# Optimization experiments

Hardware: AMD Instinct MI355X
Metric: run time of the kernel (lower is better)

The kernel has to match this reference:

```python
import jax, jax.numpy as jnp
from jax import lax
import numpy as np

LBDA = 0.1


def otam_cum_dist(dists, lbda=LBDA):
    """OTAM cumulative distance, dists: [Q, S, L, M] -> [Q, S].

    Matches the torch reference: pad last dim by 1 on each side with zeros,
    then run the banded soft-min (temperature lbda) DP recurrence. We use
    logaddexp for the stable form of -lbda*log(sum(exp(-x/lbda))).
    """
    Q, S, L, M = dists.shape
    d = jnp.pad(dists, ((0, 0), (0, 0), (0, 0), (1, 1)))  # [Q,S,L,M+2]

    # Row 0: cum[0,0]=0, cum[0,m]=sum_{k=1..m} d[0,k]  (prefix sum)
    zero_col = jnp.zeros((Q, S, 1), d.dtype)
    row0 = jnp.concatenate([zero_col, jnp.cumsum(d[:, :, 0, 1:], axis=-1)], axis=-1)

    # For m = 1 .. M+1: boundary columns (m==1 and m==M+1) add the
    # extra exp(-cum[l-1, m]/lbda) term.
    is_bnd = np.zeros(M + 1, dtype=bool)
    is_bnd[0] = True
    is_bnd[-1] = True
    is_bnd = jnp.asarray(is_bnd)

    def row_step(prev_row, d_row):
        # prev_row, d_row: [Q, S, M+2]
        def col_step(prev_cur, xs):
            d_lm, pr_m1, pr_m, bnd = xs  # each [Q,S] (bnd scalar)
            s = jnp.logaddexp(-pr_m1 / lbda, -prev_cur / lbda)
            s = jnp.where(bnd, jnp.logaddexp(s, -pr_m / lbda), s)
            cur = d_lm - lbda * s
            return cur, cur

        xs = (
            jnp.moveaxis(d_row[:, :, 1:], -1, 0),        # d[l, m],     m=1..M+1
            jnp.moveaxis(prev_row[:, :, :-1], -1, 0),    # cum[l-1,m-1]
            jnp.moveaxis(prev_row[:, :, 1:], -1, 0),     # cum[l-1,m]
            is_bnd,
        )
        zero = jnp.zeros(d_row.shape[:2], d_row.dtype)
        _, cols = lax.scan(col_step, zero, xs)           # [M+1, Q, S]
        new_row = jnp.concatenate([zero[..., None], jnp.moveaxis(cols, 0, -1)], axis=-1)
        return new_row, None

    d_rows = jnp.moveaxis(d[:, :, 1:, :], 2, 0)          # [L-1, Q, S, M+2]
    last_row, _ = lax.scan(row_step, row0, d_rows)
    return last_row[:, :, -1]


def setup_inputs() -> dict:
    key = jax.random.key(0)
    similarity = jax.random.uniform(key, (400, 400, 16, 16), dtype=jnp.float32)
    return {"similarity": similarity}


def reference(similarity):
    distance = 1.0 - similarity
    votes = otam_cum_dist(distance) + otam_cum_dist(
        jnp.transpose(distance, (0, 1, 3, 2))
    )
    votes = votes * 0.5
    return -votes
```

## Files before the change

### kernel.cpp

```cpp
#include <hip/hip_runtime.h>


#define KSC  14.426950408889634f
#define HCL2 0.034657359027997264f

#define A0 0.00013544f
#define A1 1.4369229f
#define A2 -0.67162489f
#define A3 0.31367219f
#define A4 -0.07916012f

#if __has_builtin(__builtin_amdgcn_exp2f)
static __device__ __forceinline__ float fexp2(float x) { return __builtin_amdgcn_exp2f(x); }
#else
static __device__ __forceinline__ float fexp2(float x) {
    float r; asm("v_exp_f32 %0, %1" : "=v"(r) : "v"(x)); return r;
}
#endif

static __device__ __forceinline__ float lse2(float x, float y) {
    float e = fexp2(-fabsf(x - y));
    float p = __builtin_fmaf(__builtin_fmaf(__builtin_fmaf(
                  __builtin_fmaf(A4, e, A3), e, A2), e, A1), e, A0);
    return fmaxf(x, y) + p;
}
static __device__ __forceinline__ float lse3(float x, float y, float z) {
    return lse2(lse2(x, y), z);
}

#define UNPACKK(rk, b0, b1, b2, b3)                                              \
    rk[0]=(b0.x-1.0f)*KSC;  rk[1]=(b0.y-1.0f)*KSC;  rk[2]=(b0.z-1.0f)*KSC;       \
    rk[3]=(b0.w-1.0f)*KSC;  rk[4]=(b1.x-1.0f)*KSC;  rk[5]=(b1.y-1.0f)*KSC;       \
    rk[6]=(b1.z-1.0f)*KSC;  rk[7]=(b1.w-1.0f)*KSC;  rk[8]=(b2.x-1.0f)*KSC;       \
    rk[9]=(b2.y-1.0f)*KSC;  rk[10]=(b2.z-1.0f)*KSC; rk[11]=(b2.w-1.0f)*KSC;      \
    rk[12]=(b3.x-1.0f)*KSC; rk[13]=(b3.y-1.0f)*KSC; rk[14]=(b3.z-1.0f)*KSC;      \
    rk[15]=(b3.w-1.0f)*KSC

#define PIPE_ADVANCE(l)                                                          \
    b0 = c0; b1 = c1; b2 = c2; b3 = c3;                                          \
    c0 = e0; c1 = e1; c2 = e2; c3 = e3;                                          \
    if ((l) + 2 < 16) {                                                          \
        e0 = tp[((l) + 2) * 4 + 0]; e1 = tp[((l) + 2) * 4 + 1];                  \
        e2 = tp[((l) + 2) * 4 + 2]; e3 = tp[((l) + 2) * 4 + 3];                  \
    }

__global__ __launch_bounds__(128) void otam_kernel(const float* __restrict__ sim,
                                                   float* __restrict__ out,
                                                   int npairs) {
    __shared__ float tshare[64];
    const int lane = threadIdx.x & 63;
    const int wid  = threadIdx.x >> 6;
    int p = blockIdx.x * 64 + lane;
    if (p >= npairs) p = npairs - 1;
    const float4* tp = (const float4*)(sim + (size_t)p * 256);

    float rk[16];
    float4 b0 = tp[0], b1 = tp[1], b2 = tp[2],  b3 = tp[3];
    float4 c0 = tp[4], c1 = tp[5], c2 = tp[6],  c3 = tp[7];
    float4 e0 = tp[8], e1 = tp[9], e2 = tp[10], e3 = tp[11];

    UNPACKK(rk, b0, b1, b2, b3);

    float resu;
    if (wid == 0) {
        float up[18];
        up[0] = 0.0f;
#pragma unroll
        for (int m = 1; m <= 16; ++m) up[m] = up[m - 1] + rk[m - 1];
        up[17] = up[16];

        for (int l = 1; l < 16; ++l) {
            PIPE_ADVANCE(l);
            UNPACKK(rk, b0, b1, b2, b3);
            float t   = up[1];
            float cur = lse2(1.0f, t) + rk[0];
            up[1] = cur;
            float a_old = t;
#pragma unroll
            for (int m = 2; m <= 16; ++m) {
                t      = up[m];
                cur    = lse2(a_old, cur) + rk[m - 1];
                up[m]  = cur;
                a_old  = t;
            }
            up[17] = lse3(a_old, cur, up[17]);
        }
        resu = up[17];
    } else {
        float S[16];
        {
            float cur = rk[0];
            S[0] = cur;
#pragma unroll
            for (int i = 1; i < 16; ++i) {
                cur  = lse2(1.0f, cur) + rk[i];
                S[i] = cur;
            }
        }
        for (int l = 1; l < 16; ++l) {
            PIPE_ADVANCE(l);
            UNPACKK(rk, b0, b1, b2, b3);
            float po  = S[0];
            float cur = S[0] + rk[0];
            S[0] = cur;
#pragma unroll
            for (int i = 1; i < 16; ++i) {
                float t = S[i];
                cur  = lse2(po, t) + rk[i];
                S[i] = cur;
                po   = t;
            }
        }
        {
            float po = S[0], cur = S[0];
#pragma unroll
            for (int i = 1; i < 16; ++i) {
                float t = S[i];
                cur = lse3(po, t, cur);
                po  = t;
            }
            tshare[lane] = cur;
        }
        resu = 0.0f;
    }

    __syncthreads();
    if (wid == 0) {
        out[p] = HCL2 * (resu + tshare[lane]);
    }
}

extern "C" void kernel_launch(void* const* d_in, const int* in_sizes, int n_in,
                              void* d_out, int out_size, void* d_ws, size_t ws_size,
                              hipStream_t stream) {
    const float* sim = (const float*)d_in[0];
    float* out       = (float*)d_out;
    int npairs = in_sizes[0] / 256;
    int blocks = (npairs + 63) / 64;
    otam_kernel<<<blocks, 128, 0, stream>>>(sim, out, npairs);
}
```

Measured before the change: 236.8 us.

## Stage inputs through double-buffered LDS with coalesced loads shared by both waves

Replaces per-lane strided global loads (each wave reading the full pair matrix) with cooperative coalesced float4 loads by all 128 threads into a padded, double-buffered shared memory staging area, processed two rows per chunk. This targets uncoalesced access and the duplicated global reads between the row-pass and column-pass waves. It adds a block barrier per chunk and shared memory usage, which may reduce occupancy.

```diff
diff --git a/kernel.cpp b/kernel.cpp
--- a/kernel.cpp
+++ b/kernel.cpp
@@ -28,105 +28,171 @@
     return lse2(lse2(x, y), z);
 }
 
-#define UNPACKK(rk, b0, b1, b2, b3)                                              \
-    rk[0]=(b0.x-1.0f)*KSC;  rk[1]=(b0.y-1.0f)*KSC;  rk[2]=(b0.z-1.0f)*KSC;       \
-    rk[3]=(b0.w-1.0f)*KSC;  rk[4]=(b1.x-1.0f)*KSC;  rk[5]=(b1.y-1.0f)*KSC;       \
-    rk[6]=(b1.z-1.0f)*KSC;  rk[7]=(b1.w-1.0f)*KSC;  rk[8]=(b2.x-1.0f)*KSC;       \
-    rk[9]=(b2.y-1.0f)*KSC;  rk[10]=(b2.z-1.0f)*KSC; rk[11]=(b2.w-1.0f)*KSC;      \
-    rk[12]=(b3.x-1.0f)*KSC; rk[13]=(b3.y-1.0f)*KSC; rk[14]=(b3.z-1.0f)*KSC;      \
-    rk[15]=(b3.w-1.0f)*KSC
-
-#define PIPE_ADVANCE(l)                                                          \
-    b0 = c0; b1 = c1; b2 = c2; b3 = c3;                                          \
-    c0 = e0; c1 = e1; c2 = e2; c3 = e3;                                          \
-    if ((l) + 2 < 16) {                                                          \
-        e0 = tp[((l) + 2) * 4 + 0]; e1 = tp[((l) + 2) * 4 + 1];                  \
-        e2 = tp[((l) + 2) * 4 + 2]; e3 = tp[((l) + 2) * 4 + 3];                  \
-    }
+#define UNPACKQ(rk, q)                                                         \
+    rk[0]=(q[0].x-1.0f)*KSC;  rk[1]=(q[0].y-1.0f)*KSC;                         \
+    rk[2]=(q[0].z-1.0f)*KSC;  rk[3]=(q[0].w-1.0f)*KSC;                         \
+    rk[4]=(q[1].x-1.0f)*KSC;  rk[5]=(q[1].y-1.0f)*KSC;                         \
+    rk[6]=(q[1].z-1.0f)*KSC;  rk[7]=(q[1].w-1.0f)*KSC;                         \
+    rk[8]=(q[2].x-1.0f)*KSC;  rk[9]=(q[2].y-1.0f)*KSC;                         \
+    rk[10]=(q[2].z-1.0f)*KSC; rk[11]=(q[2].w-1.0f)*KSC;                        \
+    rk[12]=(q[3].x-1.0f)*KSC; rk[13]=(q[3].y-1.0f)*KSC;                        \
+    rk[14]=(q[3].z-1.0f)*KSC; rk[15]=(q[3].w-1.0f)*KSC
 
 __global__ __launch_bounds__(128) void otam_kernel(const float* __restrict__ sim,
                                                    float* __restrict__ out,
                                                    int npairs) {
+    __shared__ float4 lds[2][64 * 9];
     __shared__ float tshare[64];
-    const int lane = threadIdx.x & 63;
-    const int wid  = threadIdx.x >> 6;
-    int p = blockIdx.x * 64 + lane;
-    if (p >= npairs) p = npairs - 1;
-    const float4* tp = (const float4*)(sim + (size_t)p * 256);
-
+    const int t    = threadIdx.x;
+    const int lane = t & 63;
+    const int wid  = t >> 6;
+    const unsigned basePair = (unsigned)blockIdx.x * 64u;
+    const float4* g = (const float4*)sim;
+    const unsigned totF4 = (unsigned)npairs * 64u;
+
+    unsigned j_[4], s_[4];
+#pragma unroll
+    for (int i = 0; i < 4; ++i) {
+        unsigned f = (unsigned)(i * 128 + t);
+        j_[i] = f >> 3; s_[i] = f & 7u;
+    }
+
+#define GLOAD(dst, c)                                                          \
+    _Pragma("unroll")                                                          \
+    for (int i = 0; i < 4; ++i) {                                              \
+        unsigned gi = (basePair + j_[i]) * 64u + (unsigned)(c) * 8u + s_[i];   \
+        gi = gi < totF4 ? gi : totF4 - 1u;                                     \
+        dst[i] = g[gi];                                                        \
+    }
+#define LDSWRITE(src, b)                                                       \
+    _Pragma("unroll")                                                          \
+    for (int i = 0; i < 4; ++i) lds[b][j_[i] * 9u + s_[i]] = src[i];
+
+    float4 stA[4], stB[4];
+    GLOAD(stA, 0);
+    GLOAD(stB, 1);
+    LDSWRITE(stA, 0);
+
+    float up[18];
+    float S[16];
     float rk[16];
-    float4 b0 = tp[0], b1 = tp[1], b2 = tp[2],  b3 = tp[3];
-    float4 c0 = tp[4], c1 = tp[5], c2 = tp[6],  c3 = tp[7];
-    float4 e0 = tp[8], e1 = tp[9], e2 = tp[10], e3 = tp[11];
-
-    UNPACKK(rk, b0, b1, b2, b3);
-
-    float resu;
-    if (wid == 0) {
-        float up[18];
-        up[0] = 0.0f;
-#pragma unroll
-        for (int m = 1; m <= 16; ++m) up[m] = up[m - 1] + rk[m - 1];
-        up[17] = up[16];
-
-        for (int l = 1; l < 16; ++l) {
-            PIPE_ADVANCE(l);
-            UNPACKK(rk, b0, b1, b2, b3);
-            float t   = up[1];
-            float cur = lse2(1.0f, t) + rk[0];
-            up[1] = cur;
-            float a_old = t;
-#pragma unroll
-            for (int m = 2; m <= 16; ++m) {
-                t      = up[m];
-                cur    = lse2(a_old, cur) + rk[m - 1];
-                up[m]  = cur;
-                a_old  = t;
-            }
-            up[17] = lse3(a_old, cur, up[17]);
-        }
-        resu = up[17];
-    } else {
-        float S[16];
-        {
-            float cur = rk[0];
-            S[0] = cur;
-#pragma unroll
-            for (int i = 1; i < 16; ++i) {
-                cur  = lse2(1.0f, cur) + rk[i];
-                S[i] = cur;
-            }
-        }
-        for (int l = 1; l < 16; ++l) {
-            PIPE_ADVANCE(l);
-            UNPACKK(rk, b0, b1, b2, b3);
-            float po  = S[0];
-            float cur = S[0] + rk[0];
-            S[0] = cur;
-#pragma unroll
-            for (int i = 1; i < 16; ++i) {
-                float t = S[i];
-                cur  = lse2(po, t) + rk[i];
-                S[i] = cur;
-                po   = t;
-            }
-        }
-        {
-            float po = S[0], cur = S[0];
-#pragma unroll
-            for (int i = 1; i < 16; ++i) {
-                float t = S[i];
-                cur = lse3(po, t, cur);
-                po  = t;
-            }
-            tshare[lane] = cur;
-        }
-        resu = 0.0f;
-    }
-
+
+#pragma unroll
+    for (int c = 0; c < 8; ++c) {
+        __syncthreads();
+
+        if (c + 2 < 8) {
+            if (c & 1) { GLOAD(stB, c + 2); } else { GLOAD(stA, c + 2); }
+        }
+
+        float4 r0q[4], r1q[4];
+#pragma unroll
+        for (int k = 0; k < 4; ++k) r0q[k] = lds[c & 1][lane * 9 + k];
+#pragma unroll
+        for (int k = 0; k < 4; ++k) r1q[k] = lds[c & 1][lane * 9 + 4 + k];
+
+        if (c + 1 < 8) {
+            if (c & 1) { LDSWRITE(stA, (c + 1) & 1); } else { LDSWRITE(stB, (c + 1) & 1); }
+        }
+
+        if (wid == 0) {
+            if (c == 0) {
+                UNPACKQ(rk, r0q);
+                up[0] = 0.0f;
+#pragma unroll
+                for (int m = 1; m <= 16; ++m) up[m] = up[m - 1] + rk[m - 1];
+                up[17] = up[16];
+                UNPACKQ(rk, r1q);
+            } else {
+                UNPACKQ(rk, r0q);
+                {
+                    float tt  = up[1];
+                    float cur = lse2(1.0f, tt) + rk[0];
+                    up[1] = cur;
+                    float a_old = tt;
+#pragma unroll
+                    for (int m = 2; m <= 16; ++m) {
+                        tt    = up[m];
+                        cur   = lse2(a_old, cur) + rk[m - 1];
+                        up[m] = cur;
+                        a_old = tt;
+                    }
+                    up[17] = lse3(a_old, cur, up[17]);
+                }
+                UNPACKQ(rk, r1q);
+            }
+            {
+                float tt  = up[1];
+                float cur = lse2(1.0f, tt) + rk[0];
+                up[1] = cur;
+                float a_old = tt;
+#pragma unroll
+                for (int m = 2; m <= 16; ++m) {
+                    tt    = up[m];
+                    cur   = lse2(a_old, cur) + rk[m - 1];
+                    up[m] = cur;
+                    a_old = tt;
+                }
+                up[17] = lse3(a_old, cur, up[17]);
+            }
+        } else {
+            if (c == 0) {
+                UNPACKQ(rk, r0q);
+                {
+                    float cur = rk[0];
+                    S[0] = cur;
+#pragma unroll
+                    for (int i = 1; i < 16; ++i) {
+                        cur  = lse2(1.0f, cur) + rk[i];
+                        S[i] = cur;
+                    }
+                }
+                UNPACKQ(rk, r1q);
+            } else {
+                UNPACKQ(rk, r0q);
+                {
+                    float po  = S[0];
+                    float cur = S[0] + rk[0];
+                    S[0] = cur;
+#pragma unroll
+                    for (int i = 1; i < 16; ++i) {
+                        float tt = S[i];
+                        cur  = lse2(po, tt) + rk[i];
+                        S[i] = cur;
+                        po   = tt;
+                    }
+                }
+                UNPACKQ(rk, r1q);
+            }
+            {
+                float po  = S[0];
+                float cur = S[0] + rk[0];
+                S[0] = cur;
+#pragma unroll
+                for (int i = 1; i < 16; ++i) {
+                    float tt = S[i];
+                    cur  = lse2(po, tt) + rk[i];
+                    S[i] = cur;
+                    po   = tt;
+                }
+            }
+        }
+    }
+
+    if (wid == 1) {
+        float po = S[0], cur = S[0];
+#pragma unroll
+        for (int i = 1; i < 16; ++i) {
+            float tt = S[i];
+            cur = lse3(po, tt, cur);
+            po  = tt;
+        }
+        tshare[lane] = cur;
+    }
     __syncthreads();
     if (wid == 0) {
-        out[p] = HCL2 * (resu + tshare[lane]);
+        unsigned p = basePair + (unsigned)lane;
+        if (p < (unsigned)npairs) out[p] = HCL2 * (up[17] + tshare[lane]);
     }
 }
 
```

After: 250.5 us. 5.8% more time.
